# Kernel tuning notes

Hardware: AMD Instinct MI355X
Metric: run time of the kernel (lower is better)

The kernel has to match this reference:

```python
import jax, jax.numpy as jnp
import numpy as np

N_EXPERTS = 8
FDIM1 = 1024
FDIM2 = 512
NUM_CLASSES = 64
BATCH = 16384


def setup_inputs() -> dict:
    key = jax.random.key(0)
    k1, k2, k3, k4, k5, k6 = jax.random.split(key, 6)
    s1 = 1.0 / np.sqrt(FDIM1)
    s2 = 1.0 / np.sqrt(FDIM2)
    return {
        "domain": jax.random.randint(k1, (BATCH,), 0, N_EXPERTS, dtype=jnp.int64 if jax.config.jax_enable_x64 else jnp.int32),
        "x": jax.random.normal(k2, (BATCH, FDIM1), dtype=jnp.float32),
        "W1": jax.random.uniform(k3, (N_EXPERTS, FDIM1, FDIM2), jnp.float32, -s1, s1),
        "b1": jax.random.uniform(k4, (N_EXPERTS, FDIM2), jnp.float32, -s1, s1),
        "W2": jax.random.uniform(k5, (N_EXPERTS, FDIM2, NUM_CLASSES), jnp.float32, -s2, s2),
        "b2": jax.random.uniform(k6, (N_EXPERTS, NUM_CLASSES), jnp.float32, -s2, s2),
    }


def reference(domain, x, W1, b1, W2, b2):
    # All-expert 2-layer MLP (matches torch loop-over-experts + stack):
    # h: [B, E, fdim2]
    h = jax.nn.relu(jnp.einsum("bf,efh->beh", x, W1) + b1[None, :, :])
    # logits: [B, E, C]
    logits = jnp.einsum("beh,ehc->bec", h, W2) + b2[None, :, :]
    # Gather the expert selected by each sample's domain, then softmax.
    sel = jnp.take_along_axis(logits, domain[:, None, None].astype(jnp.int32), axis=1)[:, 0, :]
    return jax.nn.softmax(sel, axis=-1)
```

## Files before the change

kernel.cpp:

```cpp
#include <hip/hip_runtime.h>
#include <hip/hip_bf16.h>

#define BATCH 16384
#define F1    1024
#define F2    512
#define NCLS  64
#define NEXP  8
#define BPAD  (BATCH + NEXP*128)
#define NBM   136
#define NBG1  544
#define NBG2  272

typedef __attribute__((ext_vector_type(8))) short short8;
typedef __attribute__((ext_vector_type(4))) float float4v;

#define O_META   0
#define O_BEXP   4096
#define O_ORDER  8192
#define O_XPH    131072
#define O_XPL    (O_XPH + 35651584)
#define O_W1H    (O_XPL + 35651584)
#define O_W1L    (O_W1H + 8388608)
#define O_W2H    (O_W1L + 8388608)
#define O_W2L    (O_W2H + 524288)
#define O_HH     (O_W2L + 524288)
#define O_HL     (O_HH + 17825792)

__device__ inline short bf16_rn(float f) {
    unsigned u = __builtin_bit_cast(unsigned, f);
    u = (u + 0x7fffu + ((u >> 16) & 1u)) >> 16;
    return (short)u;
}
__device__ inline float bf16_up(short h) {
    return __builtin_bit_cast(float, ((unsigned)(unsigned short)h) << 16);
}
__device__ inline void split2(float v, short& hi, short& lo) {
    hi = bf16_rn(v);
    lo = bf16_rn(v - bf16_up(hi));
}
__device__ inline float4v mfma16(short8 a, short8 b, float4v c) {
    return __builtin_amdgcn_mfma_f32_16x16x32_bf16(a, b, c, 0, 0, 0);
}
__device__ inline void glds16(const void* g, void* l) {
    __builtin_amdgcn_global_load_lds((const __attribute__((address_space(1))) void*)g,
                                     (__attribute__((address_space(3))) void*)l,
                                     16, 0, 0);
}

__global__ void dael_init(const int* __restrict__ domain, int* meta, int* order) {
    __shared__ int hc[NEXP];
    const int b = blockIdx.x, t = threadIdx.x;
    const int i = b * 256 + t;
    if (i < BPAD) order[i] = -1;
    if (b < 64) {
        if (t < NEXP) hc[t] = 0;
        __syncthreads();
        atomicAdd(&hc[domain[i]], 1);
        __syncthreads();
        if (t < NEXP) meta[64 + b * NEXP + t] = hc[t];
    }
}

__global__ void dael_plan(int* meta, int* bexp) {
    __shared__ int cnt[NEXP], soff[NEXP + 1];
    const int t = threadIdx.x;
    if (t < NEXP) {
        int s = 0;
        for (int b = 0; b < 64; ++b) s += meta[64 + b * NEXP + t];
        cnt[t] = s;
    }
    __syncthreads();
    if (t == 0) {
        int acc = 0;
        for (int e = 0; e < NEXP; ++e) {
            soff[e] = acc;
            meta[16 + e] = acc * 128;
            meta[8 + e] = 0;
            acc += (cnt[e] + 127) >> 7;
        }
        soff[NEXP] = acc;
    }
    __syncthreads();
    for (int i = t; i < NBM; i += 256) {
        int ee = -1;
        #pragma unroll
        for (int e = 0; e < NEXP; ++e)
            if (i >= soff[e] && i < soff[e + 1]) ee = e;
        bexp[i] = ee;
    }
}

__global__ void dael_scatter(const int* __restrict__ domain, int* meta, int* order) {
    __shared__ int lc[NEXP], lb[NEXP];
    const int t = threadIdx.x;
    const int i = blockIdx.x * 256 + t;
    if (t < NEXP) lc[t] = 0;
    __syncthreads();
    const int d = domain[i];
    const int r = atomicAdd(&lc[d], 1);
    __syncthreads();
    if (t < NEXP && lc[t] > 0) lb[t] = atomicAdd(&meta[8 + t], lc[t]);
    __syncthreads();
    order[meta[16 + d] + lb[d] + r] = i;
}

#define NPX 1088
#define NPW1 1024
#define NPW2 64
__global__ __launch_bounds__(256)
void dael_pack(const int* __restrict__ order,
               const float* __restrict__ x, short* xph, short* xpl,
               const float* __restrict__ W1, short* w1h, short* w1l,
               const float* __restrict__ W2, short* w2h, short* w2l) {
    const int b = blockIdx.x, t = threadIdx.x;
    if (b < NPX) {
        const int mb = b >> 3, kg = b & 7;
        const int r = t & 127;
        const int samp = order[mb * 128 + r];
        #pragma unroll
        for (int kl = 0; kl < 4; ++kl) {
            const int ks = kg * 4 + kl;
            const size_t tb = (size_t)(mb * 32 + ks) * 4096;
            #pragma unroll
            for (int sl = 0; sl < 2; ++sl) {
                const int s = t + sl * 256;
                const int q = s >> 7;
                short8 vh = {}, vl = {};
                if (samp >= 0) {
                    const float* src = x + (size_t)samp * F1 + ks * 32 + q * 8;
                    float4 f0 = *(const float4*)src;
                    float4 f1 = *(const float4*)(src + 4);
                    float va[8] = {f0.x, f0.y, f0.z, f0.w, f1.x, f1.y, f1.z, f1.w};
                    #pragma unroll
                    for (int i = 0; i < 8; ++i) { short h, l; split2(va[i], h, l); vh[i] = h; vl[i] = l; }
                }
                *(short8*)(xph + tb + s * 8) = vh;
                *(short8*)(xpl + tb + s * 8) = vl;
            }
        }
    } else if (b < NPX + NPW1) {
        const int b2 = b - NPX;
        const int e = b2 >> 7, strip = (b2 >> 5) & 3, ks = b2 & 31;
        const size_t tb = (size_t)((e * 4 + strip) * 32 + ks) * 4096;
        #pragma unroll
        for (int sl = 0; sl < 2; ++sl) {
            const int s = t + sl * 256;
            const int q = s >> 7, r = s & 127;
            const int n = strip * 128 + r;
            short8 vh, vl;
            #pragma unroll
            for (int jj = 0; jj < 8; ++jj) {
                const int k = ks * 32 + q * 8 + jj;
                float v = W1[((size_t)(e * F1 + k)) * F2 + n];
                short h, l; split2(v, h, l); vh[jj] = h; vl[jj] = l;
            }
            *(short8*)(w1h + tb + s * 8) = vh;
            *(short8*)(w1l + tb + s * 8) = vl;
        }
    } else {
        const int b3 = b - NPX - NPW1;
        const int e = b3 >> 3, ks = b3 & 7;
        const size_t tb = (size_t)(e * 8 + ks) * 4096;
        #pragma unroll
        for (int sl = 0; sl < 2; ++sl) {
            const int s = t + sl * 256;
            const int q = s >> 6, c = s & 63;
            short8 vh, vl;
            #pragma unroll
            for (int jj = 0; jj < 8; ++jj) {
                const int k = ks * 64 + q * 8 + jj;
                float v = W2[((size_t)(e * F2 + k)) * NCLS + c];
                short h, l; split2(v, h, l); vh[jj] = h; vl[jj] = l;
            }
            *(short8*)(w2h + tb + s * 8) = vh;
            *(short8*)(w2l + tb + s * 8) = vl;
        }
    }
}

__global__ __launch_bounds__(256, 4)
void dael_gemm1(const int* __restrict__ bexp,
                const short* __restrict__ xph, const short* __restrict__ xpl,
                const short* __restrict__ w1h, const short* __restrict__ w1l,
                const float* __restrict__ b1,
                short* __restrict__ hh, short* __restrict__ hl) {
    const int L = blockIdx.x;
    const int xcd = L & 7, j = L >> 3;
    const int mb = xcd * 17 + (j % 17);
    const int strip = j / 17;
    const int e = bexp[mb];
    if (e < 0) return;
    const int tid = threadIdx.x;
    const int lane = tid & 63, wv = tid >> 6;
    const int quad = lane >> 4, lrow = lane & 15;
    const int r0w = (wv & 1) * 64, c0w = (wv >> 1) * 64;

    __shared__ __align__(16) char SMc[36864];

    const size_t abase = (size_t)(mb * 32) * 4096 + (size_t)(quad * 128 + r0w + lrow) * 8;
    const short* AH = xph + abase;
    const short* AL = xpl + abase;
    const short* Bh = w1h + (size_t)((e * 4 + strip) * 32) * 4096 + tid * 8;
    const short* Bl = w1l + (size_t)((e * 4 + strip) * 32) * 4096 + tid * 8;
    const int d0 = tid * 16;

    float4v acc[4][4] = {};
    int offb[4];
    #pragma unroll
    for (int jj = 0; jj < 4; ++jj) offb[jj] = quad * 2048 + (c0w + jj * 16 + lrow) * 16;

    {
        glds16(Bh,        SMc + d0);
        glds16(Bh + 2048, SMc + 4096 + d0);
        glds16(Bl,        SMc + 8192 + d0);
        glds16(Bl + 2048, SMc + 12288 + d0);
    }

    for (int ks = 0; ks < 32; ++ks) {
        short8 ah[4], al[4];
        {
            const int sa = ks * 4096;
            #pragma unroll
            for (int i = 0; i < 4; ++i) {
                ah[i] = *(const short8*)(AH + sa + i * 128);
                al[i] = *(const short8*)(AL + sa + i * 128);
            }
        }
        __syncthreads();
        if (ks + 1 < 32) {
            const int so = (ks + 1) * 4096;
            const int dn = ((ks + 1) & 1) * 16384;
            glds16(Bh + so,        SMc + dn + d0);
            glds16(Bh + so + 2048, SMc + dn + 4096 + d0);
            glds16(Bl + so,        SMc + dn + 8192 + d0);
            glds16(Bl + so + 2048, SMc + dn + 12288 + d0);
        }
        const int db = (ks & 1) * 16384;
        __builtin_amdgcn_s_setprio(1);
        #pragma unroll
        for (int jj = 0; jj < 4; ++jj) {
            short8 bh = *(const short8*)(SMc + db + offb[jj]);
            short8 bl = *(const short8*)(SMc + db + 8192 + offb[jj]);
            #pragma unroll
            for (int i = 0; i < 4; ++i) {
                acc[i][jj] = mfma16(ah[i], bh, acc[i][jj]);
                acc[i][jj] = mfma16(ah[i], bl, acc[i][jj]);
                acc[i][jj] = mfma16(al[i], bh, acc[i][jj]);
            }
        }
        __builtin_amdgcn_s_setprio(0);
    }

    float bv[4];
    #pragma unroll
    for (int jj = 0; jj < 4; ++jj)
        bv[jj] = b1[e * F2 + strip * 128 + c0w + jj * 16 + lrow];
    short* T = (short*)SMc;
    #pragma unroll
    for (int plane = 0; plane < 2; ++plane) {
        __syncthreads();
        #pragma unroll
        for (int i = 0; i < 4; ++i)
            #pragma unroll
            for (int jj = 0; jj < 4; ++jj)
                #pragma unroll
                for (int r = 0; r < 4; ++r) {
                    const int m = r0w + i * 16 + quad * 4 + r;
                    const int n = c0w + jj * 16 + lrow;
                    float hv = fmaxf(acc[i][jj][r] + bv[jj], 0.f);
                    short hi = bf16_rn(hv);
                    T[m * 136 + n] = plane ? bf16_rn(hv - bf16_up(hi)) : hi;
                }
        __syncthreads();
        short* dst = plane ? hl : hh;
        #pragma unroll
        for (int u = 0; u < 8; ++u) {
            const int sidx = tid + 256 * u;
            const int g = sidx >> 6, m64 = sidx & 63;
            const int mloc = g >> 4, ksl = (g >> 3) & 1, q = g & 7;
            const int m = mloc * 64 + m64;
            const int n = ksl * 64 + q * 8;
            const size_t off = ((size_t)((mb * 2 + mloc) * 8 + strip * 2 + ksl)) * 4096
                               + q * 512 + m64 * 8;
            *(short8*)(dst + off) = *(const short8*)&T[m * 136 + n];
        }
    }
}

__global__ __launch_bounds__(256)
void dael_gemm2(const int* __restrict__ order, const int* __restrict__ bexp,
                const short* __restrict__ hh, const short* __restrict__ hl,
                const short* __restrict__ w2h, const short* __restrict__ w2l,
                const float* __restrict__ b2, float* __restrict__ out) {
    const int b = blockIdx.x;
    const int e = bexp[b >> 1];
    if (e < 0) return;
    const int p0 = b * 64;
    const int tid = threadIdx.x;
    const int lane = tid & 63, wv = tid >> 6;
    const int quad = lane >> 4, lrow = lane & 15;

    __shared__ __align__(16) char SM2[65536];
    __shared__ float inv[64];

    const short* Ah = hh + (size_t)(b * 8) * 4096 + tid * 8;
    const short* Al = hl + (size_t)(b * 8) * 4096 + tid * 8;
    const short* Bh = w2h + (size_t)(e * 8) * 4096 + tid * 8;
    const short* Bl = w2l + (size_t)(e * 8) * 4096 + tid * 8;
    const int d0 = tid * 16;

    float4v acc[4] = {};

    {
        glds16(Ah,        SM2 + d0);
        glds16(Ah + 2048, SM2 + 4096 + d0);
        glds16(Al,        SM2 + 8192 + d0);
        glds16(Al + 2048, SM2 + 12288 + d0);
        glds16(Bh,        SM2 + 16384 + d0);
        glds16(Bh + 2048, SM2 + 20480 + d0);
        glds16(Bl,        SM2 + 24576 + d0);
        glds16(Bl + 2048, SM2 + 28672 + d0);
    }

    for (int ks = 0; ks < 8; ++ks) {
        __syncthreads();
        if (ks + 1 < 8) {
            const int so = (ks + 1) * 4096;
            const int db = ((ks + 1) & 1) * 32768;
            glds16(Ah + so,        SM2 + db + d0);
            glds16(Ah + so + 2048, SM2 + db + 4096 + d0);
            glds16(Al + so,        SM2 + db + 8192 + d0);
            glds16(Al + so + 2048, SM2 + db + 12288 + d0);
            glds16(Bh + so,        SM2 + db + 16384 + d0);
            glds16(Bh + so + 2048, SM2 + db + 20480 + d0);
            glds16(Bl + so,        SM2 + db + 24576 + d0);
            glds16(Bl + so + 2048, SM2 + db + 28672 + d0);
        }
        const int db = (ks & 1) * 32768;
        #pragma unroll
        for (int ksub = 0; ksub < 2; ++ksub) {
            const int qa = (ksub * 4 + quad) * 1024;
            const int ao = db + qa + (wv * 16 + lrow) * 16;
            short8 ahf = *(const short8*)(SM2 + ao);
            short8 alf = *(const short8*)(SM2 + 8192 + ao);
            #pragma unroll
            for (int jj = 0; jj < 4; ++jj) {
                const int bo = db + 16384 + qa + (jj * 16 + lrow) * 16;
                short8 bh = *(const short8*)(SM2 + bo);
                short8 bl = *(const short8*)(SM2 + 8192 + bo);
                acc[jj] = mfma16(ahf, bh, acc[jj]);
                acc[jj] = mfma16(ahf, bl, acc[jj]);
                acc[jj] = mfma16(alf, bh, acc[jj]);
            }
        }
    }

    __syncthreads();
    float* Lx = (float*)SM2;
    #pragma unroll
    for (int jj = 0; jj < 4; ++jj) {
        const int n = jj * 16 + lrow;
        const float bb = b2[e * NCLS + n];
        #pragma unroll
        for (int r = 0; r < 4; ++r)
            Lx[(wv * 16 + quad * 4 + r) * 68 + n] = acc[jj][r] + bb;
    }
    __syncthreads();
    if (tid < 64) {
        float mx = -3.402823466e38f;
        #pragma unroll 8
        for (int c = 0; c < NCLS; ++c) mx = fmaxf(mx, Lx[tid * 68 + c]);
        float s = 0.f;
        #pragma unroll 8
        for (int c = 0; c < NCLS; ++c) {
            float ev = __expf(Lx[tid * 68 + c] - mx);
            Lx[tid * 68 + c] = ev; s += ev;
        }
        inv[tid] = 1.f / s;
    }
    __syncthreads();
    const int r = tid >> 2, cs = (tid & 3) * 16;
    const int samp = order[p0 + r];
    if (samp >= 0) {
        const float sc = inv[r];
        #pragma unroll
        for (int q = 0; q < 4; ++q) {
            float4 v = *(const float4*)&Lx[r * 68 + cs + q * 4];
            v.x *= sc; v.y *= sc; v.z *= sc; v.w *= sc;
            *(float4*)(out + (size_t)samp * NCLS + cs + q * 4) = v;
        }
    }
}

extern "C" void kernel_launch(void* const* d_in, const int* in_sizes, int n_in,
                              void* d_out, int out_size, void* d_ws, size_t ws_size,
                              hipStream_t stream) {
    const int*   domain = (const int*)d_in[0];
    const float* x      = (const float*)d_in[1];
    const float* W1     = (const float*)d_in[2];
    const float* b1     = (const float*)d_in[3];
    const float* W2     = (const float*)d_in[4];
    const float* b2     = (const float*)d_in[5];
    float* out = (float*)d_out;

    char* ws = (char*)d_ws;
    int*   meta  = (int*)(ws + O_META);
    int*   bexp  = (int*)(ws + O_BEXP);
    int*   order = (int*)(ws + O_ORDER);
    short* xph   = (short*)(ws + O_XPH);
    short* xpl   = (short*)(ws + O_XPL);
    short* w1h   = (short*)(ws + O_W1H);
    short* w1l   = (short*)(ws + O_W1L);
    short* w2h   = (short*)(ws + O_W2H);
    short* w2l   = (short*)(ws + O_W2L);
    short* hh    = (short*)(ws + O_HH);
    short* hl    = (short*)(ws + O_HL);

    dael_init<<<68, 256, 0, stream>>>(domain, meta, order);
    dael_plan<<<1, 256, 0, stream>>>(meta, bexp);
    dael_scatter<<<64, 256, 0, stream>>>(domain, meta, order);
    dael_pack<<<NPX + NPW1 + NPW2, 256, 0, stream>>>(order, x, xph, xpl,
                                                     W1, w1h, w1l, W2, w2h, w2l);
    dael_gemm1<<<NBG1, 256, 0, stream>>>(bexp, xph, xpl, w1h, w1l, b1, hh, hl);
    dael_gemm2<<<NBG2, 256, 0, stream>>>(order, bexp, hh, hl, w2h, w2l, b2, out);
}
```

Baseline: 236.3 us.

## Double-buffer A-operand register prefetch in gemm1 with manual vmcnt waits

Restructures the gemm1 main loop so the A-operand (x hi/lo) fragments for step k+2 are loaded into a second register set while step k's MFMAs run. The loop is manually unrolled by two, and explicit s_waitcnt vmcnt plus a raw s_barrier replace __syncthreads, so outstanding global loads are not all drained each iteration. Launch bounds drop from 4 to 3 waves per SIMD to make room for the extra registers. This lowers occupancy, and the hand-counted vmcnt values are fragile if the compiler reorders memory operations.

```diff
diff --git a/kernel.cpp b/kernel.cpp
--- a/kernel.cpp
+++ b/kernel.cpp
@@ -178,7 +178,7 @@
     }
 }
 
-__global__ __launch_bounds__(256, 4)
+__global__ __launch_bounds__(256, 3)
 void dael_gemm1(const int* __restrict__ bexp,
                 const short* __restrict__ xph, const short* __restrict__ xpl,
                 const short* __restrict__ w1h, const short* __restrict__ w1l,
@@ -209,47 +209,68 @@
     #pragma unroll
     for (int jj = 0; jj < 4; ++jj) offb[jj] = quad * 2048 + (c0w + jj * 16 + lrow) * 16;
 
-    {
-        glds16(Bh,        SMc + d0);
-        glds16(Bh + 2048, SMc + 4096 + d0);
-        glds16(Bl,        SMc + 8192 + d0);
-        glds16(Bl + 2048, SMc + 12288 + d0);
-    }
-
-    for (int ks = 0; ks < 32; ++ks) {
-        short8 ah[4], al[4];
-        {
-            const int sa = ks * 4096;
-            #pragma unroll
-            for (int i = 0; i < 4; ++i) {
-                ah[i] = *(const short8*)(AH + sa + i * 128);
-                al[i] = *(const short8*)(AL + sa + i * 128);
-            }
-        }
-        __syncthreads();
-        if (ks + 1 < 32) {
-            const int so = (ks + 1) * 4096;
-            const int dn = ((ks + 1) & 1) * 16384;
-            glds16(Bh + so,        SMc + dn + d0);
-            glds16(Bh + so + 2048, SMc + dn + 4096 + d0);
-            glds16(Bl + so,        SMc + dn + 8192 + d0);
-            glds16(Bl + so + 2048, SMc + dn + 12288 + d0);
-        }
-        const int db = (ks & 1) * 16384;
-        __builtin_amdgcn_s_setprio(1);
-        #pragma unroll
-        for (int jj = 0; jj < 4; ++jj) {
-            short8 bh = *(const short8*)(SMc + db + offb[jj]);
-            short8 bl = *(const short8*)(SMc + db + 8192 + offb[jj]);
-            #pragma unroll
-            for (int i = 0; i < 4; ++i) {
-                acc[i][jj] = mfma16(ah[i], bh, acc[i][jj]);
-                acc[i][jj] = mfma16(ah[i], bl, acc[i][jj]);
-                acc[i][jj] = mfma16(al[i], bh, acc[i][jj]);
-            }
-        }
-        __builtin_amdgcn_s_setprio(0);
-    }
+    short8 a0h[4], a0l[4], a1h[4], a1l[4];
+
+    #pragma unroll
+    for (int i = 0; i < 4; ++i) {
+        a0h[i] = *(const short8*)(AH + i * 128);
+        a0l[i] = *(const short8*)(AL + i * 128);
+    }
+    asm volatile("" ::: "memory");
+    glds16(Bh,        SMc + d0);
+    glds16(Bh + 2048, SMc + 4096 + d0);
+    glds16(Bl,        SMc + 8192 + d0);
+    glds16(Bl + 2048, SMc + 12288 + d0);
+    asm volatile("" ::: "memory");
+    #pragma unroll
+    for (int i = 0; i < 4; ++i) {
+        a1h[i] = *(const short8*)(AH + 4096 + i * 128);
+        a1l[i] = *(const short8*)(AL + 4096 + i * 128);
+    }
+
+#define G1_ITER(KS, CURH, CURL, DB, DN)                                        \
+    {                                                                          \
+        if ((KS) == 31) { asm volatile("s_waitcnt vmcnt(0)" ::: "memory"); }   \
+        else            { asm volatile("s_waitcnt vmcnt(8)" ::: "memory"); }   \
+        __builtin_amdgcn_s_barrier();                                          \
+        asm volatile("" ::: "memory");                                         \
+        if ((KS) + 1 < 32) {                                                   \
+            const int so_ = ((KS) + 1) * 4096;                                 \
+            glds16(Bh + so_,        SMc + (DN) + d0);                          \
+            glds16(Bh + so_ + 2048, SMc + (DN) + 4096 + d0);                   \
+            glds16(Bl + so_,        SMc + (DN) + 8192 + d0);                   \
+            glds16(Bl + so_ + 2048, SMc + (DN) + 12288 + d0);                  \
+        }                                                                      \
+        asm volatile("" ::: "memory");                                         \
+        __builtin_amdgcn_s_setprio(1);                                         \
+        _Pragma("unroll")                                                      \
+        for (int jj = 0; jj < 4; ++jj) {                                       \
+            short8 bh = *(const short8*)(SMc + (DB) + offb[jj]);               \
+            short8 bl = *(const short8*)(SMc + (DB) + 8192 + offb[jj]);        \
+            _Pragma("unroll")                                                  \
+            for (int i = 0; i < 4; ++i) {                                      \
+                acc[i][jj] = mfma16(CURH[i], bh, acc[i][jj]);                  \
+                acc[i][jj] = mfma16(CURH[i], bl, acc[i][jj]);                  \
+                acc[i][jj] = mfma16(CURL[i], bh, acc[i][jj]);                  \
+            }                                                                  \
+        }                                                                      \
+        __builtin_amdgcn_s_setprio(0);                                         \
+        asm volatile("" ::: "memory");                                         \
+        if ((KS) + 2 < 32) {                                                   \
+            const int sa_ = ((KS) + 2) * 4096;                                 \
+            _Pragma("unroll")                                                  \
+            for (int i = 0; i < 4; ++i) {                                      \
+                CURH[i] = *(const short8*)(AH + sa_ + i * 128);                \
+                CURL[i] = *(const short8*)(AL + sa_ + i * 128);                \
+            }                                                                  \
+        }                                                                      \
+    }
+
+    for (int kb = 0; kb < 32; kb += 2) {
+        G1_ITER(kb,     a0h, a0l, 0,     16384);
+        G1_ITER(kb + 1, a1h, a1l, 16384, 0);
+    }
+#undef G1_ITER
 
     float bv[4];
     #pragma unroll
```

Result: faster. 222.0 us (-6.0%).

## Fuse x split into gemm1, merge planning kernels, triple-buffer W1 tiles

Applied to the files above, without the earlier changes.

Drops the separate pass that packed x into hi/lo bf16 planes. gemm1 now gathers x rows through the order array and splits them into hi/lo bf16 in registers, using packed conversions. The init, plan and weight-pack kernels are merged into fewer launches, and the scatter kernel computes its prefix sums itself. gemm1 switches to a three-stage LDS ring for the W1 tiles with explicit waitcnt, and gemm2 remaps block indices across XCDs. This removes roughly 140MB of round-trip traffic for the packed x. In exchange it adds split ALU work inside the GEMM loop, uncoalesced gathered x loads, and lower occupancy (launch bounds 3, larger LDS).

```diff
diff --git a/kernel.cpp b/kernel.cpp
--- a/kernel.cpp
+++ b/kernel.cpp
@@ -13,6 +13,7 @@
 
 typedef __attribute__((ext_vector_type(8))) short short8;
 typedef __attribute__((ext_vector_type(4))) float float4v;
+typedef __attribute__((ext_vector_type(4))) unsigned uint4v;
 
 #define O_META   0
 #define O_BEXP   4096
@@ -46,101 +47,52 @@
                                      (__attribute__((address_space(3))) void*)l,
                                      16, 0, 0);
 }
-
-__global__ void dael_init(const int* __restrict__ domain, int* meta, int* order) {
+__device__ inline unsigned cvt_pk_bf16(float a, float b) {
+    __hip_bfloat162 h = __float22bfloat162_rn(make_float2(a, b));
+    union { __hip_bfloat162 v; unsigned u; } cv;
+    cv.v = h;
+    return cv.u;
+}
+__device__ inline void splitA8(const float4& r0, const float4& r1, short8& vh, short8& vl) {
+    const unsigned u0 = cvt_pk_bf16(r0.x, r0.y);
+    const unsigned u1 = cvt_pk_bf16(r0.z, r0.w);
+    const unsigned u2 = cvt_pk_bf16(r1.x, r1.y);
+    const unsigned u3 = cvt_pk_bf16(r1.z, r1.w);
+    uint4v uh = {u0, u1, u2, u3};
+    vh = __builtin_bit_cast(short8, uh);
+    const unsigned l0 = cvt_pk_bf16(r0.x - __builtin_bit_cast(float, u0 << 16),
+                                    r0.y - __builtin_bit_cast(float, u0 & 0xFFFF0000u));
+    const unsigned l1 = cvt_pk_bf16(r0.z - __builtin_bit_cast(float, u1 << 16),
+                                    r0.w - __builtin_bit_cast(float, u1 & 0xFFFF0000u));
+    const unsigned l2 = cvt_pk_bf16(r1.x - __builtin_bit_cast(float, u2 << 16),
+                                    r1.y - __builtin_bit_cast(float, u2 & 0xFFFF0000u));
+    const unsigned l3 = cvt_pk_bf16(r1.z - __builtin_bit_cast(float, u3 << 16),
+                                    r1.w - __builtin_bit_cast(float, u3 & 0xFFFF0000u));
+    uint4v ul = {l0, l1, l2, l3};
+    vl = __builtin_bit_cast(short8, ul);
+}
+
+#define NPW1 1024
+#define NPW2 64
+__global__ __launch_bounds__(256)
+void dael_init_pack(const int* __restrict__ domain, int* meta, int* order,
+                    const float* __restrict__ W1, short* w1h, short* w1l,
+                    const float* __restrict__ W2, short* w2h, short* w2l) {
     __shared__ int hc[NEXP];
     const int b = blockIdx.x, t = threadIdx.x;
-    const int i = b * 256 + t;
-    if (i < BPAD) order[i] = -1;
+    if (b < 68) {
+        const int i = b * 256 + t;
+        if (i < BPAD) order[i] = -1;
+    }
     if (b < 64) {
         if (t < NEXP) hc[t] = 0;
         __syncthreads();
-        atomicAdd(&hc[domain[i]], 1);
+        atomicAdd(&hc[domain[b * 256 + t]], 1);
         __syncthreads();
         if (t < NEXP) meta[64 + b * NEXP + t] = hc[t];
     }
-}
-
-__global__ void dael_plan(int* meta, int* bexp) {
-    __shared__ int cnt[NEXP], soff[NEXP + 1];
-    const int t = threadIdx.x;
-    if (t < NEXP) {
-        int s = 0;
-        for (int b = 0; b < 64; ++b) s += meta[64 + b * NEXP + t];
-        cnt[t] = s;
-    }
-    __syncthreads();
-    if (t == 0) {
-        int acc = 0;
-        for (int e = 0; e < NEXP; ++e) {
-            soff[e] = acc;
-            meta[16 + e] = acc * 128;
-            meta[8 + e] = 0;
-            acc += (cnt[e] + 127) >> 7;
-        }
-        soff[NEXP] = acc;
-    }
-    __syncthreads();
-    for (int i = t; i < NBM; i += 256) {
-        int ee = -1;
-        #pragma unroll
-        for (int e = 0; e < NEXP; ++e)
-            if (i >= soff[e] && i < soff[e + 1]) ee = e;
-        bexp[i] = ee;
-    }
-}
-
-__global__ void dael_scatter(const int* __restrict__ domain, int* meta, int* order) {
-    __shared__ int lc[NEXP], lb[NEXP];
-    const int t = threadIdx.x;
-    const int i = blockIdx.x * 256 + t;
-    if (t < NEXP) lc[t] = 0;
-    __syncthreads();
-    const int d = domain[i];
-    const int r = atomicAdd(&lc[d], 1);
-    __syncthreads();
-    if (t < NEXP && lc[t] > 0) lb[t] = atomicAdd(&meta[8 + t], lc[t]);
-    __syncthreads();
-    order[meta[16 + d] + lb[d] + r] = i;
-}
-
-#define NPX 1088
-#define NPW1 1024
-#define NPW2 64
-__global__ __launch_bounds__(256)
-void dael_pack(const int* __restrict__ order,
-               const float* __restrict__ x, short* xph, short* xpl,
-               const float* __restrict__ W1, short* w1h, short* w1l,
-               const float* __restrict__ W2, short* w2h, short* w2l) {
-    const int b = blockIdx.x, t = threadIdx.x;
-    if (b < NPX) {
-        const int mb = b >> 3, kg = b & 7;
-        const int r = t & 127;
-        const int samp = order[mb * 128 + r];
-        #pragma unroll
-        for (int kl = 0; kl < 4; ++kl) {
-            const int ks = kg * 4 + kl;
-            const size_t tb = (size_t)(mb * 32 + ks) * 4096;
-            #pragma unroll
-            for (int sl = 0; sl < 2; ++sl) {
-                const int s = t + sl * 256;
-                const int q = s >> 7;
-                short8 vh = {}, vl = {};
-                if (samp >= 0) {
-                    const float* src = x + (size_t)samp * F1 + ks * 32 + q * 8;
-                    float4 f0 = *(const float4*)src;
-                    float4 f1 = *(const float4*)(src + 4);
-                    float va[8] = {f0.x, f0.y, f0.z, f0.w, f1.x, f1.y, f1.z, f1.w};
-                    #pragma unroll
-                    for (int i = 0; i < 8; ++i) { short h, l; split2(va[i], h, l); vh[i] = h; vl[i] = l; }
-                }
-                *(short8*)(xph + tb + s * 8) = vh;
-                *(short8*)(xpl + tb + s * 8) = vl;
-            }
-        }
-    } else if (b < NPX + NPW1) {
-        const int b2 = b - NPX;
-        const int e = b2 >> 7, strip = (b2 >> 5) & 3, ks = b2 & 31;
+    if (b < NPW1) {
+        const int e = b >> 7, strip = (b >> 5) & 3, ks = b & 31;
         const size_t tb = (size_t)((e * 4 + strip) * 32 + ks) * 4096;
         #pragma unroll
         for (int sl = 0; sl < 2; ++sl) {
@@ -158,7 +110,7 @@
             *(short8*)(w1l + tb + s * 8) = vl;
         }
     } else {
-        const int b3 = b - NPX - NPW1;
+        const int b3 = b - NPW1;
         const int e = b3 >> 3, ks = b3 & 7;
         const size_t tb = (size_t)(e * 8 + ks) * 4096;
         #pragma unroll
@@ -178,9 +130,55 @@
     }
 }
 
-__global__ __launch_bounds__(256, 4)
-void dael_gemm1(const int* __restrict__ bexp,
-                const short* __restrict__ xph, const short* __restrict__ xpl,
+__global__ __launch_bounds__(256)
+void dael_scatter(const int* __restrict__ domain, const int* __restrict__ meta,
+                  int* order, int* bexp) {
+    __shared__ int hist[64 * NEXP];
+    __shared__ int pre[NEXP], base[NEXP], soff[NEXP + 1], lc[NEXP];
+    const int b = blockIdx.x, t = threadIdx.x;
+    if (t < NEXP) lc[t] = 0;
+    for (int idx = t; idx < 64 * NEXP; idx += 256) hist[idx] = meta[64 + idx];
+    __syncthreads();
+    if (t < NEXP) {
+        int c = 0, p = 0;
+        for (int bb = 0; bb < 64; ++bb) {
+            const int h = hist[bb * NEXP + t];
+            c += h;
+            if (bb < b) p += h;
+        }
+        pre[t] = p;
+        hist[t] = c;
+    }
+    __syncthreads();
+    if (t == 0) {
+        int acc = 0;
+        #pragma unroll
+        for (int e = 0; e < NEXP; ++e) {
+            soff[e] = acc;
+            base[e] = acc * 128;
+            acc += (hist[e] + 127) >> 7;
+        }
+        soff[NEXP] = acc;
+    }
+    __syncthreads();
+    const int i = b * 256 + t;
+    const int d = domain[i];
+    const int r = atomicAdd(&lc[d], 1);
+    order[base[d] + pre[d] + r] = i;
+    if (b == 0) {
+        for (int k = t; k < NBM; k += 256) {
+            int ee = -1;
+            #pragma unroll
+            for (int e = 0; e < NEXP; ++e)
+                if (k >= soff[e] && k < soff[e + 1]) ee = e;
+            bexp[k] = ee;
+        }
+    }
+}
+
+__global__ __launch_bounds__(256, 3)
+void dael_gemm1(const int* __restrict__ order, const int* __restrict__ bexp,
+                const float* __restrict__ x,
                 const short* __restrict__ w1h, const short* __restrict__ w1l,
                 const float* __restrict__ b1,
                 short* __restrict__ hh, short* __restrict__ hl) {
@@ -195,11 +193,15 @@
     const int quad = lane >> 4, lrow = lane & 15;
     const int r0w = (wv & 1) * 64, c0w = (wv >> 1) * 64;
 
-    __shared__ __align__(16) char SMc[36864];
-
-    const size_t abase = (size_t)(mb * 32) * 4096 + (size_t)(quad * 128 + r0w + lrow) * 8;
-    const short* AH = xph + abase;
-    const short* AL = xpl + abase;
+    __shared__ __align__(16) char SMc[49152];
+
+    const float* xb[4];
+    #pragma unroll
+    for (int i = 0; i < 4; ++i) {
+        int s = order[mb * 128 + r0w + i * 16 + lrow];
+        if (s < 0) s = 0;
+        xb[i] = x + (size_t)s * F1 + quad * 8;
+    }
     const short* Bh = w1h + (size_t)((e * 4 + strip) * 32) * 4096 + tid * 8;
     const short* Bl = w1l + (size_t)((e * 4 + strip) * 32) * 4096 + tid * 8;
     const int d0 = tid * 16;
@@ -209,38 +211,54 @@
     #pragma unroll
     for (int jj = 0; jj < 4; ++jj) offb[jj] = quad * 2048 + (c0w + jj * 16 + lrow) * 16;
 
-    {
-        glds16(Bh,        SMc + d0);
-        glds16(Bh + 2048, SMc + 4096 + d0);
-        glds16(Bl,        SMc + 8192 + d0);
-        glds16(Bl + 2048, SMc + 12288 + d0);
-    }
+    float4 ra[4][2];
+    int c0 = 0, c1 = 16384, c2 = 32768;
+
+    #pragma unroll
+    for (int i = 0; i < 4; ++i) {
+        ra[i][0] = *(const float4*)(xb[i]);
+        ra[i][1] = *(const float4*)(xb[i] + 4);
+    }
+    asm volatile("" ::: "memory");
+    glds16(Bh,        SMc + d0);
+    glds16(Bh + 2048, SMc + 4096 + d0);
+    glds16(Bl,        SMc + 8192 + d0);
+    glds16(Bl + 2048, SMc + 12288 + d0);
+    glds16(Bh + 4096,        SMc + 16384 + d0);
+    glds16(Bh + 4096 + 2048, SMc + 16384 + 4096 + d0);
+    glds16(Bl + 4096,        SMc + 16384 + 8192 + d0);
+    glds16(Bl + 4096 + 2048, SMc + 16384 + 12288 + d0);
 
     for (int ks = 0; ks < 32; ++ks) {
+        if (ks == 31) { asm volatile("s_waitcnt vmcnt(0)" ::: "memory"); }
+        else          { asm volatile("s_waitcnt vmcnt(4)" ::: "memory"); }
+        __builtin_amdgcn_s_barrier();
+        asm volatile("" ::: "memory");
         short8 ah[4], al[4];
-        {
-            const int sa = ks * 4096;
+        #pragma unroll
+        for (int i = 0; i < 4; ++i) splitA8(ra[i][0], ra[i][1], ah[i], al[i]);
+        if (ks + 1 < 32) {
+            const int ao = (ks + 1) * 32;
             #pragma unroll
             for (int i = 0; i < 4; ++i) {
-                ah[i] = *(const short8*)(AH + sa + i * 128);
-                al[i] = *(const short8*)(AL + sa + i * 128);
+                ra[i][0] = *(const float4*)(xb[i] + ao);
+                ra[i][1] = *(const float4*)(xb[i] + ao + 4);
             }
         }
-        __syncthreads();
-        if (ks + 1 < 32) {
-            const int so = (ks + 1) * 4096;
-            const int dn = ((ks + 1) & 1) * 16384;
-            glds16(Bh + so,        SMc + dn + d0);
-            glds16(Bh + so + 2048, SMc + dn + 4096 + d0);
-            glds16(Bl + so,        SMc + dn + 8192 + d0);
-            glds16(Bl + so + 2048, SMc + dn + 12288 + d0);
-        }
-        const int db = (ks & 1) * 16384;
+        asm volatile("" ::: "memory");
+        if (ks + 2 < 32) {
+            const int so = (ks + 2) * 4096;
+            glds16(Bh + so,        SMc + c2 + d0);
+            glds16(Bh + so + 2048, SMc + c2 + 4096 + d0);
+            glds16(Bl + so,        SMc + c2 + 8192 + d0);
+            glds16(Bl + so + 2048, SMc + c2 + 12288 + d0);
+        }
+        __builtin_amdgcn_sched_barrier(0);
         __builtin_amdgcn_s_setprio(1);
         #pragma unroll
         for (int jj = 0; jj < 4; ++jj) {
-            short8 bh = *(const short8*)(SMc + db + offb[jj]);
-            short8 bl = *(const short8*)(SMc + db + 8192 + offb[jj]);
+            short8 bh = *(const short8*)(SMc + c0 + offb[jj]);
+            short8 bl = *(const short8*)(SMc + c0 + 8192 + offb[jj]);
             #pragma unroll
             for (int i = 0; i < 4; ++i) {
                 acc[i][jj] = mfma16(ah[i], bh, acc[i][jj]);
@@ -249,6 +267,7 @@
             }
         }
         __builtin_amdgcn_s_setprio(0);
+        const int tmp = c0; c0 = c1; c1 = c2; c2 = tmp;
     }
 
     float bv[4];
@@ -292,7 +311,8 @@
                 const short* __restrict__ hh, const short* __restrict__ hl,
                 const short* __restrict__ w2h, const short* __restrict__ w2l,
                 const float* __restrict__ b2, float* __restrict__ out) {
-    const int b = blockIdx.x;
+    const int L = blockIdx.x;
+    const int b = (L & 7) * 34 + (L >> 3);
     const int e = bexp[b >> 1];
     if (e < 0) return;
     const int p0 = b * 64;
@@ -407,8 +427,6 @@
     int*   meta  = (int*)(ws + O_META);
     int*   bexp  = (int*)(ws + O_BEXP);
     int*   order = (int*)(ws + O_ORDER);
-    short* xph   = (short*)(ws + O_XPH);
-    short* xpl   = (short*)(ws + O_XPL);
     short* w1h   = (short*)(ws + O_W1H);
     short* w1l   = (short*)(ws + O_W1L);
     short* w2h   = (short*)(ws + O_W2H);
@@ -416,11 +434,9 @@
     short* hh    = (short*)(ws + O_HH);
     short* hl    = (short*)(ws + O_HL);
 
-    dael_init<<<68, 256, 0, stream>>>(domain, meta, order);
-    dael_plan<<<1, 256, 0, stream>>>(meta, bexp);
-    dael_scatter<<<64, 256, 0, stream>>>(domain, meta, order);
-    dael_pack<<<NPX + NPW1 + NPW2, 256, 0, stream>>>(order, x, xph, xpl,
-                                                     W1, w1h, w1l, W2, w2h, w2l);
-    dael_gemm1<<<NBG1, 256, 0, stream>>>(bexp, xph, xpl, w1h, w1l, b1, hh, hl);
+    dael_init_pack<<<NPW1 + NPW2, 256, 0, stream>>>(domain, meta, order,
+                                                    W1, w1h, w1l, W2, w2h, w2l);
+    dael_scatter<<<64, 256, 0, stream>>>(domain, meta, order, bexp);
+    dael_gemm1<<<NBG1, 256, 0, stream>>>(order, bexp, x, w1h, w1l, b1, hh, hl);
     dael_gemm2<<<NBG2, 256, 0, stream>>>(order, bexp, hh, hl, w2h, w2l, b2, out);
 }
```

Result: no change. 240.1 us (+1.6%).
